# Kernel tuning notes

Measured on AMD Instinct MI355X. Metric: run time of the kernel, lower is better.

Reference implementation:

```python
import jax, jax.numpy as jnp
import numpy as np

N_NODES = 100000
N_EDGES = 3200000
D_FEAT = 256
HIDDEN = 16


def setup_inputs() -> dict:
    key = jax.random.key(0)
    k1, k2, k3, k4 = jax.random.split(key, 4)
    x = jax.random.normal(k1, (N_NODES, D_FEAT), dtype=jnp.float32)
    edge_index = jax.random.randint(k2, (2, N_EDGES), 0, N_NODES, dtype=jnp.int64)
    # GCNConv linear weight (Glorot-ish scale) and bias
    W = jax.random.normal(k3, (D_FEAT, HIDDEN), dtype=jnp.float32) / np.sqrt(D_FEAT)
    b_conv = jnp.zeros((HIDDEN,), dtype=jnp.float32)
    W_fc = jax.random.normal(k4, (HIDDEN, 1), dtype=jnp.float32) / np.sqrt(HIDDEN)
    b_fc = jnp.zeros((1,), dtype=jnp.float32)
    return {"x": x, "edge_index": edge_index, "W": W, "b_conv": b_conv,
            "W_fc": W_fc, "b_fc": b_fc}


def reference(x, edge_index, W, b_conv, W_fc, b_fc):
    N = x.shape[0]
    # --- GCNConv: add self-loops, symmetric normalization, transform, scatter-add ---
    loop = jnp.arange(N, dtype=edge_index.dtype)
    src = jnp.concatenate([edge_index[0], loop])  # message sources (x_j)
    dst = jnp.concatenate([edge_index[1], loop])  # aggregation targets
    # degree of target nodes (edge weights = 1, self-loops included)
    deg = jax.ops.segment_sum(jnp.ones_like(dst, dtype=x.dtype), dst, num_segments=N)
    dinv = jnp.where(deg > 0, jax.lax.rsqrt(deg), 0.0)
    norm = dinv[src] * dinv[dst]  # [E+N]
    h = x @ W                       # [N, hidden] transform before propagation
    msg = h[src] * norm[:, None]    # gather + scale
    agg = jax.ops.segment_sum(msg, dst, num_segments=N)  # scatter-add
    out = agg + b_conv
    return out @ W_fc + b_fc
```

## Files before the change

### kernel.cpp

```cpp
#include <hip/hip_runtime.h>

#define DF 256
#define HID 16
#define WB 512
#define PBITS 8
#define PMAX 512
#define PPAD 512

__global__ void __launch_bounds__(512)
hist_sval_kernel(const float* __restrict__ x, const int* __restrict__ dst,
                 const float* __restrict__ Wm, const float* __restrict__ W_fc,
                 unsigned* __restrict__ cntS, float* __restrict__ sv,
                 int N, int E, int P, int Epw) {
    __shared__ unsigned h[PMAX];
    for (int i = threadIdx.x; i < P; i += 512) h[i] = 0u;
    __syncthreads();
    const int w = blockIdx.x;
    const size_t e0 = (size_t)w * Epw;
    long rem = (long)E - (long)e0;
    int m = rem < 0 ? 0 : (rem > Epw ? Epw : (int)rem);
    int i = threadIdx.x;
    for (; i + 1536 < m; i += 2048) {
        unsigned d0 = (unsigned)dst[e0 + i];
        unsigned d1 = (unsigned)dst[e0 + i + 512];
        unsigned d2 = (unsigned)dst[e0 + i + 1024];
        unsigned d3 = (unsigned)dst[e0 + i + 1536];
        atomicAdd(&h[d0 >> PBITS], 1u); atomicAdd(&h[d1 >> PBITS], 1u);
        atomicAdd(&h[d2 >> PBITS], 1u); atomicAdd(&h[d3 >> PBITS], 1u);
    }
    for (; i < m; i += 512) atomicAdd(&h[((unsigned)dst[e0 + i]) >> PBITS], 1u);
    __syncthreads();
    for (int p = threadIdx.x; p < P; p += 512) cntS[(size_t)w * PPAD + p] = h[p];

    const int lane = threadIdx.x & 63, wid = threadIdx.x >> 6;
    const int gw = w * 8 + wid;
    const int GW = WB * 8;
    float a0 = 0.f, a1 = 0.f, a2 = 0.f, a3 = 0.f;
    {
        const float* wrow = Wm + (size_t)(lane * 4) * HID;
#pragma unroll
        for (int k = 0; k < HID; ++k) {
            float f = W_fc[k];
            a0 += wrow[k] * f;
            a1 += wrow[HID + k] * f;
            a2 += wrow[2 * HID + k] * f;
            a3 += wrow[3 * HID + k] * f;
        }
    }
    for (int r0 = gw; r0 < N; r0 += 4 * GW) {
        int r1 = r0 + GW, r2 = r0 + 2 * GW, r3 = r0 + 3 * GW;
        float4 v0, v1, v2, v3;
        v0 = reinterpret_cast<const float4*>(x + (size_t)r0 * DF)[lane];
        if (r1 < N) v1 = reinterpret_cast<const float4*>(x + (size_t)r1 * DF)[lane];
        if (r2 < N) v2 = reinterpret_cast<const float4*>(x + (size_t)r2 * DF)[lane];
        if (r3 < N) v3 = reinterpret_cast<const float4*>(x + (size_t)r3 * DF)[lane];
        float s0 = v0.x * a0 + v0.y * a1 + v0.z * a2 + v0.w * a3;
        float s1 = (r1 < N) ? (v1.x * a0 + v1.y * a1 + v1.z * a2 + v1.w * a3) : 0.f;
        float s2 = (r2 < N) ? (v2.x * a0 + v2.y * a1 + v2.z * a2 + v2.w * a3) : 0.f;
        float s3 = (r3 < N) ? (v3.x * a0 + v3.y * a1 + v3.z * a2 + v3.w * a3) : 0.f;
#pragma unroll
        for (int off = 32; off > 0; off >>= 1) {
            s0 += __shfl_xor(s0, off, 64);
            s1 += __shfl_xor(s1, off, 64);
            s2 += __shfl_xor(s2, off, 64);
            s3 += __shfl_xor(s3, off, 64);
        }
        if (lane == 0) {
            sv[r0] = s0;
            if (r1 < N) sv[r1] = s1;
            if (r2 < N) sv[r2] = s2;
            if (r3 < N) sv[r3] = s3;
        }
    }
}

__global__ void __launch_bounds__(WB)
rowscan_kernel(unsigned* __restrict__ cntS, unsigned* __restrict__ rowTotal) {
    __shared__ unsigned wsum[8];
    const int p = blockIdx.x, t = threadIdx.x;
    const int lane = t & 63, wv = t >> 6;
    unsigned v = cntS[(size_t)t * PPAD + p];
    unsigned xi = v;
#pragma unroll
    for (int off = 1; off < 64; off <<= 1) {
        unsigned u = __shfl_up(xi, off, 64);
        if (lane >= off) xi += u;
    }
    if (lane == 63) wsum[wv] = xi;
    __syncthreads();
    if (t < 8) {
        unsigned u = wsum[t];
#pragma unroll
        for (int off = 1; off < 8; off <<= 1) {
            unsigned uu = __shfl_up(u, off, 64);
            if (t >= off) u += uu;
        }
        wsum[t] = u;
    }
    __syncthreads();
    unsigned base = wv ? wsum[wv - 1] : 0u;
    cntS[(size_t)t * PPAD + p] = xi - v + base;
    if (t == 0) rowTotal[p] = wsum[7];
}

__global__ void __launch_bounds__(512)
partscan_kernel(const unsigned* __restrict__ rowTotal, unsigned* __restrict__ partBase,
                int P, int E) {
    __shared__ unsigned wsum[8];
    const int t = threadIdx.x, lane = t & 63, wv = t >> 6;
    unsigned v = (t < P) ? rowTotal[t] : 0u;
    unsigned xi = v;
#pragma unroll
    for (int off = 1; off < 64; off <<= 1) {
        unsigned u = __shfl_up(xi, off, 64);
        if (lane >= off) xi += u;
    }
    if (lane == 63) wsum[wv] = xi;
    __syncthreads();
    if (t < 8) {
        unsigned u = wsum[t];
#pragma unroll
        for (int off = 1; off < 8; off <<= 1) {
            unsigned uu = __shfl_up(u, off, 64);
            if (t >= off) u += uu;
        }
        wsum[t] = u;
    }
    __syncthreads();
    unsigned base = wv ? wsum[wv - 1] : 0u;
    if (t < P) partBase[t] = xi - v + base;
    if (t == 0) partBase[P] = (unsigned)E;
}

__global__ void __launch_bounds__(512)
binscatter_kernel(const int* __restrict__ src, const int* __restrict__ dst,
                  const unsigned* __restrict__ cntS, const unsigned* __restrict__ partBase,
                  unsigned* __restrict__ sorted, int P, int E, int Epw) {
    __shared__ unsigned cur[PMAX];
    const int w = blockIdx.x;
    for (int p = threadIdx.x; p < P; p += 512)
        cur[p] = partBase[p] + cntS[(size_t)w * PPAD + p];
    __syncthreads();
    const size_t e0 = (size_t)w * Epw;
    long rem = (long)E - (long)e0;
    int m = rem < 0 ? 0 : (rem > Epw ? Epw : (int)rem);
    int i = threadIdx.x;
    for (; i + 1536 < m; i += 2048) {
        unsigned s0 = (unsigned)src[e0 + i],        d0 = (unsigned)dst[e0 + i];
        unsigned s1 = (unsigned)src[e0 + i + 512],  d1 = (unsigned)dst[e0 + i + 512];
        unsigned s2 = (unsigned)src[e0 + i + 1024], d2 = (unsigned)dst[e0 + i + 1024];
        unsigned s3 = (unsigned)src[e0 + i + 1536], d3 = (unsigned)dst[e0 + i + 1536];
        unsigned t0 = atomicAdd(&cur[d0 >> PBITS], 1u);
        unsigned t1 = atomicAdd(&cur[d1 >> PBITS], 1u);
        unsigned t2 = atomicAdd(&cur[d2 >> PBITS], 1u);
        unsigned t3 = atomicAdd(&cur[d3 >> PBITS], 1u);
        sorted[t0] = (s0 << PBITS) | (d0 & 255u);
        sorted[t1] = (s1 << PBITS) | (d1 & 255u);
        sorted[t2] = (s2 << PBITS) | (d2 & 255u);
        sorted[t3] = (s3 << PBITS) | (d3 & 255u);
    }
    for (; i < m; i += 512) {
        unsigned s = (unsigned)src[e0 + i], d = (unsigned)dst[e0 + i];
        unsigned slot = atomicAdd(&cur[d >> PBITS], 1u);
        sorted[slot] = (s << PBITS) | (d & 255u);
    }
}

__global__ void __launch_bounds__(1024)
degfin_kernel(const unsigned* __restrict__ sorted, const unsigned* __restrict__ partBase,
              const float* __restrict__ sv, float* __restrict__ dinv,
              float* __restrict__ tval, int N) {
    __shared__ unsigned dc[256];
    const int p = blockIdx.x, t = threadIdx.x;
    if (t < 256) dc[t] = 0u;
    __syncthreads();
    const unsigned b0 = partBase[p], b1 = partBase[p + 1];
    unsigned j = b0 + t;
    for (; j + 3072 < b1; j += 4096) {
        unsigned e0 = sorted[j], e1 = sorted[j + 1024], e2 = sorted[j + 2048], e3 = sorted[j + 3072];
        atomicAdd(&dc[e0 & 255u], 1u); atomicAdd(&dc[e1 & 255u], 1u);
        atomicAdd(&dc[e2 & 255u], 1u); atomicAdd(&dc[e3 & 255u], 1u);
    }
    for (; j < b1; j += 1024) atomicAdd(&dc[sorted[j] & 255u], 1u);
    __syncthreads();
    if (t < 256) {
        int i = (p << PBITS) + t;
        if (i < N) {
            float deg = 1.0f + (float)dc[t];
            float di = rsqrtf(deg);
            dinv[i] = di;
            tval[i] = sv[i] * di;
        }
    }
}

__global__ void __launch_bounds__(1024)
reduce_kernel(const unsigned* __restrict__ sorted, const unsigned* __restrict__ partBase,
              const float* __restrict__ tval, const float* __restrict__ dinv,
              const float* __restrict__ b_conv, const float* __restrict__ W_fc,
              const float* __restrict__ b_fc, float* __restrict__ out, int N) {
    __shared__ float facc[256];
    const int p = blockIdx.x, t = threadIdx.x;
    if (t < 256) facc[t] = 0.f;
    __syncthreads();
    const unsigned b0 = partBase[p], b1 = partBase[p + 1];
    unsigned j = b0 + t;
    for (; j + 3072 < b1; j += 4096) {
        unsigned e0 = sorted[j], e1 = sorted[j + 1024], e2 = sorted[j + 2048], e3 = sorted[j + 3072];
        float v0 = tval[e0 >> PBITS], v1 = tval[e1 >> PBITS];
        float v2 = tval[e2 >> PBITS], v3 = tval[e3 >> PBITS];
        atomicAdd(&facc[e0 & 255u], v0); atomicAdd(&facc[e1 & 255u], v1);
        atomicAdd(&facc[e2 & 255u], v2); atomicAdd(&facc[e3 & 255u], v3);
    }
    for (; j < b1; j += 1024) {
        unsigned e = sorted[j];
        atomicAdd(&facc[e & 255u], tval[e >> PBITS]);
    }
    __syncthreads();
    if (t < 256) {
        int i = (p << PBITS) + t;
        if (i < N) {
            float c = 0.f;
#pragma unroll
            for (int k = 0; k < HID; ++k) c += b_conv[k] * W_fc[k];
            float di = dinv[i];
            out[i] = di * (tval[i] + facc[t]) + c + b_fc[0];
        }
    }
}

__global__ void fb_sval(const float* __restrict__ x, const float* __restrict__ Wm,
                        const float* __restrict__ W_fc, float* __restrict__ sv, int N) {
    __shared__ float wl[DF];
    int k = threadIdx.x;
    float a = 0.f;
#pragma unroll
    for (int j = 0; j < HID; ++j) a += Wm[k * HID + j] * W_fc[j];
    wl[k] = a;
    __syncthreads();
    int lane = threadIdx.x & 63, wid = threadIdx.x >> 6;
    float4 wv = reinterpret_cast<const float4*>(wl)[lane];
    for (int row = blockIdx.x * 4 + wid; row < N; row += gridDim.x * 4) {
        float4 xv = reinterpret_cast<const float4*>(x + (size_t)row * DF)[lane];
        float acc = xv.x * wv.x + xv.y * wv.y + xv.z * wv.z + xv.w * wv.w;
#pragma unroll
        for (int off = 32; off > 0; off >>= 1) acc += __shfl_xor(acc, off, 64);
        if (lane == 0) sv[row] = acc;
    }
}
__global__ void fb_count(const int* __restrict__ dst, unsigned* __restrict__ cnt, int E) {
    int stride = gridDim.x * blockDim.x;
    for (int e = blockIdx.x * blockDim.x + threadIdx.x; e < E; e += stride)
        atomicAdd(&cnt[dst[e]], 1u);
}
__global__ void fb_node(const unsigned* __restrict__ cnt, const float* __restrict__ sv,
                        const float* __restrict__ b_conv, const float* __restrict__ W_fc,
                        const float* __restrict__ b_fc, float* __restrict__ dinv,
                        float* __restrict__ tval, float* __restrict__ out, int N) {
    int i = blockIdx.x * blockDim.x + threadIdx.x;
    if (i < N) {
        float c = 0.f;
#pragma unroll
        for (int j = 0; j < HID; ++j) c += b_conv[j] * W_fc[j];
        float deg = 1.0f + (float)cnt[i];
        float di = rsqrtf(deg);
        float s = sv[i];
        dinv[i] = di; tval[i] = s * di;
        out[i] = s / deg + c + b_fc[0];
    }
}
__global__ void fb_scatter(const int* __restrict__ src, const int* __restrict__ dst,
                           const float* __restrict__ tval, const float* __restrict__ dinv,
                           float* __restrict__ out, int E) {
    int stride = gridDim.x * blockDim.x;
    for (int e = blockIdx.x * blockDim.x + threadIdx.x; e < E; e += stride) {
        int si = src[e], di = dst[e];
        atomicAdd(&out[di], tval[si] * dinv[di]);
    }
}

extern "C" void kernel_launch(void* const* d_in, const int* in_sizes, int n_in,
                              void* d_out, int out_size, void* d_ws, size_t ws_size,
                              hipStream_t stream) {
    const float* x      = (const float*)d_in[0];
    const int*   ei     = (const int*)d_in[1];
    const float* Wm     = (const float*)d_in[2];
    const float* b_conv = (const float*)d_in[3];
    const float* W_fc   = (const float*)d_in[4];
    const float* b_fc   = (const float*)d_in[5];
    float* out = (float*)d_out;

    const int N = in_sizes[0] / DF;
    const int E = in_sizes[1] / 2;
    const int* src = ei;
    const int* dst = ei + E;

    const int P   = (N + 255) >> PBITS;
    const int Epw = (E + WB - 1) / WB;

    char* ws = (char*)d_ws;
    float* sv   = (float*)ws;
    float* dinv = sv + N;
    float* tval = dinv + N;
    unsigned* cntS     = (unsigned*)(tval + N);
    unsigned* rowTotal = cntS + (size_t)WB * PPAD;
    unsigned* partBase = rowTotal + 512;
    unsigned* sorted   = partBase + 520;

    const size_t need = ((size_t)3 * N + (size_t)WB * PPAD + 512 + 520 + (size_t)E) * 4;

    if (P >= 1 && P <= PMAX && N <= (1 << 23) && ws_size >= need) {
        hist_sval_kernel<<<WB, 512, 0, stream>>>(x, dst, Wm, W_fc, cntS, sv, N, E, P, Epw);
        rowscan_kernel<<<P, WB, 0, stream>>>(cntS, rowTotal);
        partscan_kernel<<<1, 512, 0, stream>>>(rowTotal, partBase, P, E);
        binscatter_kernel<<<WB, 512, 0, stream>>>(src, dst, cntS, partBase, sorted, P, E, Epw);
        degfin_kernel<<<P, 1024, 0, stream>>>(sorted, partBase, sv, dinv, tval, N);
        reduce_kernel<<<P, 1024, 0, stream>>>(sorted, partBase, tval, dinv,
                                              b_conv, W_fc, b_fc, out, N);
    } else {
        unsigned* fcnt = (unsigned*)(tval + N);
        hipMemsetAsync(fcnt, 0, (size_t)N * 4, stream);
        fb_sval<<<2048, 256, 0, stream>>>(x, Wm, W_fc, sv, N);
        fb_count<<<2048, 256, 0, stream>>>(dst, fcnt, E);
        fb_node<<<(N + 255) / 256, 256, 0, stream>>>(fcnt, sv, b_conv, W_fc, b_fc, dinv, tval, out, N);
        fb_scatter<<<2048, 256, 0, stream>>>(src, dst, tval, dinv, out, E);
    }
}
```

Before: 84.97 us.

## Use fixed-capacity partition buckets to drop partition scan and vectorize edge loads

Each destination partition now gets a fixed-capacity slot (four times the average count, rounded up to 4096) in the sorted buffer. This removes the partscan kernel launch and the partBase lookups, and the row scan writes absolute offsets directly. The edge-list reads in the histogram, bin-scatter, degree and reduce kernels become 128-bit int4/uint4 loads, with the per-block edge count rounded up to a multiple of four so the vector accesses stay aligned. The trade-off is that a partition holding more than the capacity overflows into its neighbour with no check. The int4 reads on dst also assume E is a multiple of four.

```diff
diff --git a/kernel.cpp b/kernel.cpp
--- a/kernel.cpp
+++ b/kernel.cpp
@@ -19,16 +19,17 @@
     const size_t e0 = (size_t)w * Epw;
     long rem = (long)E - (long)e0;
     int m = rem < 0 ? 0 : (rem > Epw ? Epw : (int)rem);
-    int i = threadIdx.x;
-    for (; i + 1536 < m; i += 2048) {
-        unsigned d0 = (unsigned)dst[e0 + i];
-        unsigned d1 = (unsigned)dst[e0 + i + 512];
-        unsigned d2 = (unsigned)dst[e0 + i + 1024];
-        unsigned d3 = (unsigned)dst[e0 + i + 1536];
-        atomicAdd(&h[d0 >> PBITS], 1u); atomicAdd(&h[d1 >> PBITS], 1u);
-        atomicAdd(&h[d2 >> PBITS], 1u); atomicAdd(&h[d3 >> PBITS], 1u);
-    }
-    for (; i < m; i += 512) atomicAdd(&h[((unsigned)dst[e0 + i]) >> PBITS], 1u);
+    const int m4 = m >> 2;
+    const int4* d4 = reinterpret_cast<const int4*>(dst + e0);
+    for (int iv = threadIdx.x; iv < m4; iv += 512) {
+        int4 d = d4[iv];
+        atomicAdd(&h[((unsigned)d.x) >> PBITS], 1u);
+        atomicAdd(&h[((unsigned)d.y) >> PBITS], 1u);
+        atomicAdd(&h[((unsigned)d.z) >> PBITS], 1u);
+        atomicAdd(&h[((unsigned)d.w) >> PBITS], 1u);
+    }
+    for (int i = (m4 << 2) + threadIdx.x; i < m; i += 512)
+        atomicAdd(&h[((unsigned)dst[e0 + i]) >> PBITS], 1u);
     __syncthreads();
     for (int p = threadIdx.x; p < P; p += 512) cntS[(size_t)w * PPAD + p] = h[p];
 
@@ -75,7 +76,7 @@
 }
 
 __global__ void __launch_bounds__(WB)
-rowscan_kernel(unsigned* __restrict__ cntS, unsigned* __restrict__ rowTotal) {
+rowscan_kernel(unsigned* __restrict__ cntS, unsigned* __restrict__ rowTotal, unsigned cap) {
     __shared__ unsigned wsum[8];
     const int p = blockIdx.x, t = threadIdx.x;
     const int lane = t & 63, wv = t >> 6;
@@ -99,67 +100,38 @@
     }
     __syncthreads();
     unsigned base = wv ? wsum[wv - 1] : 0u;
-    cntS[(size_t)t * PPAD + p] = xi - v + base;
+    cntS[(size_t)t * PPAD + p] = xi - v + base + (unsigned)p * cap;
     if (t == 0) rowTotal[p] = wsum[7];
-}
-
-__global__ void __launch_bounds__(512)
-partscan_kernel(const unsigned* __restrict__ rowTotal, unsigned* __restrict__ partBase,
-                int P, int E) {
-    __shared__ unsigned wsum[8];
-    const int t = threadIdx.x, lane = t & 63, wv = t >> 6;
-    unsigned v = (t < P) ? rowTotal[t] : 0u;
-    unsigned xi = v;
-#pragma unroll
-    for (int off = 1; off < 64; off <<= 1) {
-        unsigned u = __shfl_up(xi, off, 64);
-        if (lane >= off) xi += u;
-    }
-    if (lane == 63) wsum[wv] = xi;
-    __syncthreads();
-    if (t < 8) {
-        unsigned u = wsum[t];
-#pragma unroll
-        for (int off = 1; off < 8; off <<= 1) {
-            unsigned uu = __shfl_up(u, off, 64);
-            if (t >= off) u += uu;
-        }
-        wsum[t] = u;
-    }
-    __syncthreads();
-    unsigned base = wv ? wsum[wv - 1] : 0u;
-    if (t < P) partBase[t] = xi - v + base;
-    if (t == 0) partBase[P] = (unsigned)E;
 }
 
 __global__ void __launch_bounds__(512)
 binscatter_kernel(const int* __restrict__ src, const int* __restrict__ dst,
-                  const unsigned* __restrict__ cntS, const unsigned* __restrict__ partBase,
-                  unsigned* __restrict__ sorted, int P, int E, int Epw) {
+                  const unsigned* __restrict__ cntS, unsigned* __restrict__ sorted,
+                  int P, int E, int Epw) {
     __shared__ unsigned cur[PMAX];
     const int w = blockIdx.x;
     for (int p = threadIdx.x; p < P; p += 512)
-        cur[p] = partBase[p] + cntS[(size_t)w * PPAD + p];
+        cur[p] = cntS[(size_t)w * PPAD + p];
     __syncthreads();
     const size_t e0 = (size_t)w * Epw;
     long rem = (long)E - (long)e0;
     int m = rem < 0 ? 0 : (rem > Epw ? Epw : (int)rem);
-    int i = threadIdx.x;
-    for (; i + 1536 < m; i += 2048) {
-        unsigned s0 = (unsigned)src[e0 + i],        d0 = (unsigned)dst[e0 + i];
-        unsigned s1 = (unsigned)src[e0 + i + 512],  d1 = (unsigned)dst[e0 + i + 512];
-        unsigned s2 = (unsigned)src[e0 + i + 1024], d2 = (unsigned)dst[e0 + i + 1024];
-        unsigned s3 = (unsigned)src[e0 + i + 1536], d3 = (unsigned)dst[e0 + i + 1536];
-        unsigned t0 = atomicAdd(&cur[d0 >> PBITS], 1u);
-        unsigned t1 = atomicAdd(&cur[d1 >> PBITS], 1u);
-        unsigned t2 = atomicAdd(&cur[d2 >> PBITS], 1u);
-        unsigned t3 = atomicAdd(&cur[d3 >> PBITS], 1u);
-        sorted[t0] = (s0 << PBITS) | (d0 & 255u);
-        sorted[t1] = (s1 << PBITS) | (d1 & 255u);
-        sorted[t2] = (s2 << PBITS) | (d2 & 255u);
-        sorted[t3] = (s3 << PBITS) | (d3 & 255u);
-    }
-    for (; i < m; i += 512) {
+    const int m4 = m >> 2;
+    const int4* s4 = reinterpret_cast<const int4*>(src + e0);
+    const int4* d4 = reinterpret_cast<const int4*>(dst + e0);
+    for (int iv = threadIdx.x; iv < m4; iv += 512) {
+        int4 s = s4[iv];
+        int4 d = d4[iv];
+        unsigned t0 = atomicAdd(&cur[((unsigned)d.x) >> PBITS], 1u);
+        unsigned t1 = atomicAdd(&cur[((unsigned)d.y) >> PBITS], 1u);
+        unsigned t2 = atomicAdd(&cur[((unsigned)d.z) >> PBITS], 1u);
+        unsigned t3 = atomicAdd(&cur[((unsigned)d.w) >> PBITS], 1u);
+        sorted[t0] = ((unsigned)s.x << PBITS) | ((unsigned)d.x & 255u);
+        sorted[t1] = ((unsigned)s.y << PBITS) | ((unsigned)d.y & 255u);
+        sorted[t2] = ((unsigned)s.z << PBITS) | ((unsigned)d.z & 255u);
+        sorted[t3] = ((unsigned)s.w << PBITS) | ((unsigned)d.w & 255u);
+    }
+    for (int i = (m4 << 2) + threadIdx.x; i < m; i += 512) {
         unsigned s = (unsigned)src[e0 + i], d = (unsigned)dst[e0 + i];
         unsigned slot = atomicAdd(&cur[d >> PBITS], 1u);
         sorted[slot] = (s << PBITS) | (d & 255u);
@@ -167,21 +139,24 @@
 }
 
 __global__ void __launch_bounds__(1024)
-degfin_kernel(const unsigned* __restrict__ sorted, const unsigned* __restrict__ partBase,
+degfin_kernel(const unsigned* __restrict__ sorted, const unsigned* __restrict__ rowTotal,
               const float* __restrict__ sv, float* __restrict__ dinv,
-              float* __restrict__ tval, int N) {
+              float* __restrict__ tval, int N, unsigned cap) {
     __shared__ unsigned dc[256];
     const int p = blockIdx.x, t = threadIdx.x;
     if (t < 256) dc[t] = 0u;
     __syncthreads();
-    const unsigned b0 = partBase[p], b1 = partBase[p + 1];
-    unsigned j = b0 + t;
-    for (; j + 3072 < b1; j += 4096) {
-        unsigned e0 = sorted[j], e1 = sorted[j + 1024], e2 = sorted[j + 2048], e3 = sorted[j + 3072];
-        atomicAdd(&dc[e0 & 255u], 1u); atomicAdd(&dc[e1 & 255u], 1u);
-        atomicAdd(&dc[e2 & 255u], 1u); atomicAdd(&dc[e3 & 255u], 1u);
-    }
-    for (; j < b1; j += 1024) atomicAdd(&dc[sorted[j] & 255u], 1u);
+    const unsigned cnt = rowTotal[p];
+    const unsigned b0 = (unsigned)p * cap;
+    const unsigned nv = cnt >> 2;
+    const uint4* v4 = reinterpret_cast<const uint4*>(sorted + b0);
+    for (unsigned iv = t; iv < nv; iv += 1024) {
+        uint4 v = v4[iv];
+        atomicAdd(&dc[v.x & 255u], 1u); atomicAdd(&dc[v.y & 255u], 1u);
+        atomicAdd(&dc[v.z & 255u], 1u); atomicAdd(&dc[v.w & 255u], 1u);
+    }
+    for (unsigned j = (nv << 2) + t; j < cnt; j += 1024)
+        atomicAdd(&dc[sorted[b0 + j] & 255u], 1u);
     __syncthreads();
     if (t < 256) {
         int i = (p << PBITS) + t;
@@ -195,25 +170,27 @@
 }
 
 __global__ void __launch_bounds__(1024)
-reduce_kernel(const unsigned* __restrict__ sorted, const unsigned* __restrict__ partBase,
+reduce_kernel(const unsigned* __restrict__ sorted, const unsigned* __restrict__ rowTotal,
               const float* __restrict__ tval, const float* __restrict__ dinv,
               const float* __restrict__ b_conv, const float* __restrict__ W_fc,
-              const float* __restrict__ b_fc, float* __restrict__ out, int N) {
+              const float* __restrict__ b_fc, float* __restrict__ out, int N, unsigned cap) {
     __shared__ float facc[256];
     const int p = blockIdx.x, t = threadIdx.x;
     if (t < 256) facc[t] = 0.f;
     __syncthreads();
-    const unsigned b0 = partBase[p], b1 = partBase[p + 1];
-    unsigned j = b0 + t;
-    for (; j + 3072 < b1; j += 4096) {
-        unsigned e0 = sorted[j], e1 = sorted[j + 1024], e2 = sorted[j + 2048], e3 = sorted[j + 3072];
-        float v0 = tval[e0 >> PBITS], v1 = tval[e1 >> PBITS];
-        float v2 = tval[e2 >> PBITS], v3 = tval[e3 >> PBITS];
-        atomicAdd(&facc[e0 & 255u], v0); atomicAdd(&facc[e1 & 255u], v1);
-        atomicAdd(&facc[e2 & 255u], v2); atomicAdd(&facc[e3 & 255u], v3);
-    }
-    for (; j < b1; j += 1024) {
-        unsigned e = sorted[j];
+    const unsigned cnt = rowTotal[p];
+    const unsigned b0 = (unsigned)p * cap;
+    const unsigned nv = cnt >> 2;
+    const uint4* v4 = reinterpret_cast<const uint4*>(sorted + b0);
+    for (unsigned iv = t; iv < nv; iv += 1024) {
+        uint4 v = v4[iv];
+        float f0 = tval[v.x >> PBITS], f1 = tval[v.y >> PBITS];
+        float f2 = tval[v.z >> PBITS], f3 = tval[v.w >> PBITS];
+        atomicAdd(&facc[v.x & 255u], f0); atomicAdd(&facc[v.y & 255u], f1);
+        atomicAdd(&facc[v.z & 255u], f2); atomicAdd(&facc[v.w & 255u], f3);
+    }
+    for (unsigned j = (nv << 2) + t; j < cnt; j += 1024) {
+        unsigned e = sorted[b0 + j];
         atomicAdd(&facc[e & 255u], tval[e >> PBITS]);
     }
     __syncthreads();
@@ -296,7 +273,9 @@
     const int* dst = ei + E;
 
     const int P   = (N + 255) >> PBITS;
-    const int Epw = (E + WB - 1) / WB;
+    const int Epw = (((E + WB - 1) / WB) + 3) & ~3;
+    const unsigned avg = (unsigned)((E + P - 1) / P);
+    const unsigned cap = ((4u * avg) + 4095u) & ~4095u;
 
     char* ws = (char*)d_ws;
     float* sv   = (float*)ws;
@@ -304,19 +283,17 @@
     float* tval = dinv + N;
     unsigned* cntS     = (unsigned*)(tval + N);
     unsigned* rowTotal = cntS + (size_t)WB * PPAD;
-    unsigned* partBase = rowTotal + 512;
-    unsigned* sorted   = partBase + 520;
-
-    const size_t need = ((size_t)3 * N + (size_t)WB * PPAD + 512 + 520 + (size_t)E) * 4;
+    unsigned* sorted   = rowTotal + 512;
+
+    const size_t need = ((size_t)3 * N + (size_t)WB * PPAD + 512 + (size_t)P * cap) * 4;
 
     if (P >= 1 && P <= PMAX && N <= (1 << 23) && ws_size >= need) {
         hist_sval_kernel<<<WB, 512, 0, stream>>>(x, dst, Wm, W_fc, cntS, sv, N, E, P, Epw);
-        rowscan_kernel<<<P, WB, 0, stream>>>(cntS, rowTotal);
-        partscan_kernel<<<1, 512, 0, stream>>>(rowTotal, partBase, P, E);
-        binscatter_kernel<<<WB, 512, 0, stream>>>(src, dst, cntS, partBase, sorted, P, E, Epw);
-        degfin_kernel<<<P, 1024, 0, stream>>>(sorted, partBase, sv, dinv, tval, N);
-        reduce_kernel<<<P, 1024, 0, stream>>>(sorted, partBase, tval, dinv,
-                                              b_conv, W_fc, b_fc, out, N);
+        rowscan_kernel<<<P, WB, 0, stream>>>(cntS, rowTotal, cap);
+        binscatter_kernel<<<WB, 512, 0, stream>>>(src, dst, cntS, sorted, P, E, Epw);
+        degfin_kernel<<<P, 1024, 0, stream>>>(sorted, rowTotal, sv, dinv, tval, N, cap);
+        reduce_kernel<<<P, 1024, 0, stream>>>(sorted, rowTotal, tval, dinv,
+                                              b_conv, W_fc, b_fc, out, N, cap);
     } else {
         unsigned* fcnt = (unsigned*)(tval + N);
         hipMemsetAsync(fcnt, 0, (size_t)N * 4, stream);
```

Result: faster. 82.79 us (-2.6%).
